# Optimization experiments

Measured on AMD Instinct MI355X. Metric: run time of the kernel, lower is better.

The kernel has to match this reference:

```python
import jax, jax.numpy as jnp
import numpy as np
import math

N_FREQ = 10
N_FRAGMENTS = 4_000_000
CELL_N = 2000
GENE_N = 1000
EMB_DIM = N_FREQ * 2 * 2  # 40


def setup_inputs() -> dict:
    key = jax.random.key(0)
    k1, k2, k3, k4 = jax.random.split(key, 4)
    coords = jax.random.normal(k1, (N_FRAGMENTS, 2), dtype=jnp.float32)
    ix = jnp.sort(jax.random.randint(k2, (N_FRAGMENTS,), 0, CELL_N * GENE_N, dtype=jnp.int32))
    # buffers, exactly as in FragmentEmbedder.__init__
    freqs = np.array([[1.0 / 100.0 ** (2.0 * i / N_FREQ)] * 2 for i in range(1, N_FREQ + 1)],
                     dtype=np.float32).reshape(-1)  # [2*n_freq]
    shifts = np.array([[0.0, math.pi / 2.0] for _ in range(1, N_FREQ + 1)],
                      dtype=np.float32).reshape(-1)  # [2*n_freq]
    # params (weight1 is zero-init in the original; use small random so output is non-trivial)
    weight1 = jax.random.normal(k3, (1, EMB_DIM), dtype=jnp.float32) * 0.02
    bias1 = jax.random.normal(k4, (GENE_N,), dtype=jnp.float32)  # mean_gene_expression
    return {
        "fragment_coordinates": coords,
        "fragment_cellxgene_ix": ix,
        "cell_n": CELL_N,
        "gene_n": GENE_N,
        "gene_ix": jnp.arange(GENE_N, dtype=jnp.int32),
        "frequencies": jnp.asarray(freqs),
        "shifts": jnp.asarray(shifts),
        "weight1": weight1,
        "bias1": bias1,
    }


def reference(fragment_coordinates, fragment_cellxgene_ix, cell_n, gene_n, gene_ix,
              frequencies, shifts, weight1, bias1):
    F = fragment_coordinates.shape[0]
    # sinusoidal fragment embedding: [F, 2, 2*n_freq] -> [F, 4*n_freq]
    emb = jnp.sin(fragment_coordinates[..., None] * frequencies + shifts).reshape(F, -1)
    # sorted segment sum into cell x gene buckets
    pooled = jax.ops.segment_sum(emb, fragment_cellxgene_ix,
                                 num_segments=cell_n * gene_n,
                                 indices_are_sorted=True)
    cell_gene_embedding = pooled.reshape(cell_n, gene_n, emb.shape[-1])
    # einsum 'abc,bc->ab' with weight1 of shape (1, C) == contraction over C only
    expression = jnp.einsum("abc,c->ab", cell_gene_embedding, weight1[0]) + bias1[gene_ix]
    return expression
```

## Files before the change

kernel.cpp:

```cpp
#include <hip/hip_runtime.h>
#include <math.h>

#define NFREQ 10
#define INV2PI 0.15915494309189535f
#define TPB 256
#define FPT 2
#define SCALE_F 1048576.0f
#define INV_SCALE 9.5367431640625e-07f

typedef float v2f __attribute__((ext_vector_type(2)));

__device__ float g_fr[NFREQ];
__device__ v2f   g_P[NFREQ];
__device__ v2f   g_R[NFREQ];

__device__ __forceinline__ v2f mkv2(float a, float b) { v2f r; r.x = a; r.y = b; return r; }

__global__ __launch_bounds__(256) void init_kernel(int* __restrict__ acc, int total,
                                                   const float* __restrict__ freqs,
                                                   const float* __restrict__ weight) {
    if (blockIdx.x == 0 && threadIdx.x < NFREQ) {
        int i = threadIdx.x;
        g_fr[i] = freqs[2 * i] * INV2PI;
        float A0 = weight[2 * i],             B0 = weight[2 * i + 1];
        float A1 = weight[2 * NFREQ + 2 * i], B1 = weight[2 * NFREQ + 2 * i + 1];
        g_R[i] = mkv2(sqrtf(A0 * A0 + B0 * B0), sqrtf(A1 * A1 + B1 * B1));
        g_P[i] = mkv2(atan2f(B0, A0) * INV2PI, atan2f(B1, A1) * INV2PI);
    }
    int b = (blockIdx.x * blockDim.x + threadIdx.x) * 4;
    if (b + 3 < total) {
        *(int4*)(acc + b) = make_int4(0, 0, 0, 0);
    } else {
        for (int k = 0; k < 4; ++k)
            if (b + k < total) acc[b + k] = 0;
    }
}

__device__ __forceinline__ float frag_eval(v2f c, const float* __restrict__ fr,
                                           const v2f* __restrict__ P,
                                           const v2f* __restrict__ R) {
    v2f acc = mkv2(0.f, 0.f);
#pragma unroll
    for (int i = 0; i < NFREQ; ++i) {
        v2f th = c * fr[i] + P[i];
        v2f s;
        s.x = __builtin_amdgcn_sinf(th.x);
        s.y = __builtin_amdgcn_sinf(th.y);
        acc += R[i] * s;
    }
    return acc.x + acc.y;
}

__global__ __launch_bounds__(TPB) void scan_kernel(
        const float* __restrict__ coords,
        const int*   __restrict__ ix,
        int* __restrict__ acc,
        int F) {
    float fr[NFREQ]; v2f P[NFREQ], R[NFREQ];
#pragma unroll
    for (int i = 0; i < NFREQ; ++i) {
        fr[i] = g_fr[i]; P[i] = g_P[i]; R[i] = g_R[i];
    }

    const int t  = blockIdx.x * TPB + threadIdx.x;
    const int f0 = 2 * t;
    const int lane = threadIdx.x & 63;

    int   ka = -2, kb = -3;
    float sa = 0.f, sb = 0.f;
    if (f0 + 1 < F) {
        int2   k2 = *(const int2*)(ix + f0);
        float4 c4 = *(const float4*)(coords + 2 * f0);
        ka = k2.x; kb = k2.y;
        sa = frag_eval(mkv2(c4.x, c4.y), fr, P, R);
        sb = frag_eval(mkv2(c4.z, c4.w), fr, P, R);
    } else if (f0 < F) {
        ka = ix[f0];
        float2 c2 = *(const float2*)(coords + 2 * f0);
        sa = frag_eval(mkv2(c2.x, c2.y), fr, P, R);
    }

    const bool pure = (ka == kb);
    float v = pure ? (sa + sb) : sa;

#pragma unroll
    for (int d = 1; d < 64; d <<= 1) {
        float ov = __shfl_down(v, d);
        int   ok = __shfl_down(ka, d);
        if (lane + d < 64 && ok == ka) v += ov;
    }

    const float nv  = __shfl_down(v, 1);
    const int   nk  = __shfl_down(ka, 1);
    const int   pkb = __shfl_up(kb, 1);

    const bool headA = (ka >= 0) && (lane == 0 || ka != pkb);
    if (headA)
        atomicAdd(acc + ka, __float2int_rn(v * SCALE_F));

    if (kb >= 0 && !pure) {
        float tb = sb + ((lane < 63 && nk == kb) ? nv : 0.f);
        atomicAdd(acc + kb, __float2int_rn(tb * SCALE_F));
    }
}

__global__ __launch_bounds__(256) void finish_kernel(
        float* out, const float* __restrict__ bias,
        const int* __restrict__ gix, int gene_n, int total) {
    int b = (blockIdx.x * blockDim.x + threadIdx.x) * 4;
    if ((gene_n & 3) == 0 && b + 3 < total) {
        int4 a = *(const int4*)((const int*)out + b);
        int g = b % gene_n;
        float4 r;
        r.x = bias[gix[g]]     + (float)a.x * INV_SCALE;
        r.y = bias[gix[g + 1]] + (float)a.y * INV_SCALE;
        r.z = bias[gix[g + 2]] + (float)a.z * INV_SCALE;
        r.w = bias[gix[g + 3]] + (float)a.w * INV_SCALE;
        *(float4*)(out + b) = r;
    } else {
        for (int k = 0; k < 4; ++k) {
            int j = b + k;
            if (j < total) {
                int aj = ((const int*)out)[j];
                out[j] = bias[gix[j % gene_n]] + (float)aj * INV_SCALE;
            }
        }
    }
}

extern "C" void kernel_launch(void* const* d_in, const int* in_sizes, int n_in,
                              void* d_out, int out_size, void* d_ws, size_t ws_size,
                              hipStream_t stream) {
    const float* coords  = (const float*)d_in[0];
    const int*   ix      = (const int*)d_in[1];
    const int*   gene_ix = (const int*)d_in[4];
    const float* freqs   = (const float*)d_in[5];
    const float* weight  = (const float*)d_in[7];
    const float* bias    = (const float*)d_in[8];
    float* out = (float*)d_out;

    int F      = in_sizes[1];
    int gene_n = in_sizes[4];
    int total  = out_size;

    (void)d_ws; (void)ws_size; (void)n_in;

    int zthreads = (total + 3) / 4;
    hipLaunchKernelGGL(init_kernel, dim3((zthreads + 255) / 256), dim3(256),
                       0, stream, (int*)out, total, freqs, weight);

    int blocks = (F + TPB * FPT - 1) / (TPB * FPT);
    hipLaunchKernelGGL(scan_kernel, dim3(blocks), dim3(TPB), 0, stream,
                       coords, ix, (int*)out, F);

    hipLaunchKernelGGL(finish_kernel, dim3((zthreads + 255) / 256), dim3(256),
                       0, stream, out, bias, gene_ix, gene_n, total);
}
```

Measured before the change: 110.5 us.

## Fuse zero-init, accumulation and bias epilogue into one atomic-free scan kernel

Drops the zero-fill and finish kernels and the integer atomics. Each wavefront owns a contiguous run of 128 sorted fragments and writes final bias-plus-sum values directly, including the empty cells between keys. A segment that spans wavefront boundaries is written only by the wavefront holding its first... rather, by the lane that sees its end, which walks backwards over earlier fragments and re-evaluates them. This avoids the 8MB memset and the read-modify-write pass, but adds serial gap-fill loops and occasional recomputation in a single lane.

```diff
diff --git a/kernel.cpp b/kernel.cpp
--- a/kernel.cpp
+++ b/kernel.cpp
@@ -4,9 +4,6 @@
 #define NFREQ 10
 #define INV2PI 0.15915494309189535f
 #define TPB 256
-#define FPT 2
-#define SCALE_F 1048576.0f
-#define INV_SCALE 9.5367431640625e-07f
 
 typedef float v2f __attribute__((ext_vector_type(2)));
 
@@ -16,23 +13,15 @@
 
 __device__ __forceinline__ v2f mkv2(float a, float b) { v2f r; r.x = a; r.y = b; return r; }
 
-__global__ __launch_bounds__(256) void init_kernel(int* __restrict__ acc, int total,
-                                                   const float* __restrict__ freqs,
-                                                   const float* __restrict__ weight) {
-    if (blockIdx.x == 0 && threadIdx.x < NFREQ) {
-        int i = threadIdx.x;
+__global__ void coeff_kernel(const float* __restrict__ freqs,
+                             const float* __restrict__ weight) {
+    int i = threadIdx.x;
+    if (i < NFREQ) {
         g_fr[i] = freqs[2 * i] * INV2PI;
         float A0 = weight[2 * i],             B0 = weight[2 * i + 1];
         float A1 = weight[2 * NFREQ + 2 * i], B1 = weight[2 * NFREQ + 2 * i + 1];
         g_R[i] = mkv2(sqrtf(A0 * A0 + B0 * B0), sqrtf(A1 * A1 + B1 * B1));
         g_P[i] = mkv2(atan2f(B0, A0) * INV2PI, atan2f(B1, A1) * INV2PI);
-    }
-    int b = (blockIdx.x * blockDim.x + threadIdx.x) * 4;
-    if (b + 3 < total) {
-        *(int4*)(acc + b) = make_int4(0, 0, 0, 0);
-    } else {
-        for (int k = 0; k < 4; ++k)
-            if (b + k < total) acc[b + k] = 0;
     }
 }
 
@@ -54,19 +43,27 @@
 __global__ __launch_bounds__(TPB) void scan_kernel(
         const float* __restrict__ coords,
         const int*   __restrict__ ix,
-        int* __restrict__ acc,
-        int F) {
+        const float* __restrict__ bias,
+        const int*   __restrict__ gix,
+        float* __restrict__ out,
+        int gene_n, int total, int F) {
     float fr[NFREQ]; v2f P[NFREQ], R[NFREQ];
 #pragma unroll
     for (int i = 0; i < NFREQ; ++i) {
         fr[i] = g_fr[i]; P[i] = g_P[i]; R[i] = g_R[i];
     }
 
-    const int t  = blockIdx.x * TPB + threadIdx.x;
-    const int f0 = 2 * t;
+    const int w    = (blockIdx.x * TPB + threadIdx.x) >> 6;
     const int lane = threadIdx.x & 63;
+    const int b    = w << 7;
+    if (b >= F) return;
+    const int e  = min(b + 128, F);
+    const int pk = (b > 0) ? ix[b - 1] : -1;
+    const int nk = (e < F) ? ix[e] : 0x7fffffff;
+    const int lk = ix[e - 1];
 
-    int   ka = -2, kb = -3;
+    const int f0 = b + 2 * lane;
+    int   ka = -2, kb = -2;
     float sa = 0.f, sb = 0.f;
     if (f0 + 1 < F) {
         int2   k2 = *(const int2*)(ix + f0);
@@ -75,56 +72,49 @@
         sa = frag_eval(mkv2(c4.x, c4.y), fr, P, R);
         sb = frag_eval(mkv2(c4.z, c4.w), fr, P, R);
     } else if (f0 < F) {
-        ka = ix[f0];
+        ka = kb = ix[f0];
         float2 c2 = *(const float2*)(coords + 2 * f0);
         sa = frag_eval(mkv2(c2.x, c2.y), fr, P, R);
     }
 
     const bool pure = (ka == kb);
     float v = pure ? (sa + sb) : sa;
-
 #pragma unroll
     for (int d = 1; d < 64; d <<= 1) {
         float ov = __shfl_down(v, d);
         int   ok = __shfl_down(ka, d);
         if (lane + d < 64 && ok == ka) v += ov;
     }
-
     const float nv  = __shfl_down(v, 1);
-    const int   nk  = __shfl_down(ka, 1);
+    const int   nkl = __shfl_down(ka, 1);
     const int   pkb = __shfl_up(kb, 1);
 
-    const bool headA = (ka >= 0) && (lane == 0 || ka != pkb);
-    if (headA)
-        atomicAdd(acc + ka, __float2int_rn(v * SCALE_F));
-
-    if (kb >= 0 && !pure) {
-        float tb = sb + ((lane < 63 && nk == kb) ? nv : 0.f);
-        atomicAdd(acc + kb, __float2int_rn(tb * SCALE_F));
+    if (ka >= 0 && (lane == 0 || ka != pkb)) {
+        const int Pk = (lane == 0) ? pk : pkb;
+        for (int K2 = Pk + 1; K2 < ka; ++K2)
+            out[K2] = bias[gix[K2 % gene_n]];
+        if (!(ka == lk && lk == nk)) {
+            float tot = v;
+            if (lane == 0 && ka == pk) {
+                for (int j = b - 1; j >= 0 && ix[j] == ka; --j) {
+                    float2 c2 = *(const float2*)(coords + 2 * j);
+                    tot += frag_eval(mkv2(c2.x, c2.y), fr, P, R);
+                }
+            }
+            out[ka] = bias[gix[ka % gene_n]] + tot;
+        }
     }
-}
-
-__global__ __launch_bounds__(256) void finish_kernel(
-        float* out, const float* __restrict__ bias,
-        const int* __restrict__ gix, int gene_n, int total) {
-    int b = (blockIdx.x * blockDim.x + threadIdx.x) * 4;
-    if ((gene_n & 3) == 0 && b + 3 < total) {
-        int4 a = *(const int4*)((const int*)out + b);
-        int g = b % gene_n;
-        float4 r;
-        r.x = bias[gix[g]]     + (float)a.x * INV_SCALE;
-        r.y = bias[gix[g + 1]] + (float)a.y * INV_SCALE;
-        r.z = bias[gix[g + 2]] + (float)a.z * INV_SCALE;
-        r.w = bias[gix[g + 3]] + (float)a.w * INV_SCALE;
-        *(float4*)(out + b) = r;
-    } else {
-        for (int k = 0; k < 4; ++k) {
-            int j = b + k;
-            if (j < total) {
-                int aj = ((const int*)out)[j];
-                out[j] = bias[gix[j % gene_n]] + (float)aj * INV_SCALE;
-            }
+    if (kb >= 0 && kb != ka) {
+        for (int K2 = ka + 1; K2 < kb; ++K2)
+            out[K2] = bias[gix[K2 % gene_n]];
+        if (!(kb == lk && lk == nk)) {
+            float tb = sb + ((lane < 63 && nkl == kb) ? nv : 0.f);
+            out[kb] = bias[gix[kb % gene_n]] + tb;
         }
+    }
+    if (e == F && lane == 0) {
+        for (int K2 = lk + 1; K2 < total; ++K2)
+            out[K2] = bias[gix[K2 % gene_n]];
     }
 }
 
@@ -145,14 +135,10 @@
 
     (void)d_ws; (void)ws_size; (void)n_in;
 
-    int zthreads = (total + 3) / 4;
-    hipLaunchKernelGGL(init_kernel, dim3((zthreads + 255) / 256), dim3(256),
-                       0, stream, (int*)out, total, freqs, weight);
+    hipLaunchKernelGGL(coeff_kernel, dim3(1), dim3(64), 0, stream,
+                       freqs, weight);
 
-    int blocks = (F + TPB * FPT - 1) / (TPB * FPT);
+    int blocks = (F + TPB * 2 - 1) / (TPB * 2);
     hipLaunchKernelGGL(scan_kernel, dim3(blocks), dim3(TPB), 0, stream,
-                       coords, ix, (int*)out, F);
-
-    hipLaunchKernelGGL(finish_kernel, dim3((zthreads + 255) / 256), dim3(256),
-                       0, stream, out, bias, gene_ix, gene_n, total);
+                       coords, ix, bias, gene_ix, out, gene_n, total, F);
 }
```

Result: slower. 122.7 us (+11.1%).
